# Kernel tuning notes

Measured on AMD Instinct MI355X. Metric: run time of the kernel, lower is better.

Reference implementation:

```python
import jax, jax.numpy as jnp
import numpy as np

N = 50000       # nodes
E = 1600000     # edges (avg degree 32)
DIN = 64
DOUT = 64
DE = 16
ATT_SLOPE = 0.2   # leaky_relu slope inside attention (GAT standard)
ACT_SLOPE = 0.01  # F.leaky_relu default between layers


def setup_inputs() -> dict:
    key = jax.random.key(0)
    ks = jax.random.split(key, 16)

    def lin(k, i, o):
        return jax.random.normal(k, (i, o), jnp.float32) / np.sqrt(i).astype(np.float32)

    def vec(k, d):
        return jax.random.normal(k, (d,), jnp.float32) / np.sqrt(d).astype(np.float32)

    return {
        "X": jax.random.normal(ks[0], (N, DIN), jnp.float32),
        "edge_index": jax.random.randint(ks[1], (2, E), 0, N),
        "edge_attr": jax.random.normal(ks[2], (E, DE), jnp.float32),
        # layer 1 params
        "W1": lin(ks[3], DIN, DOUT), "We1": lin(ks[4], DE, DOUT),
        "as1": vec(ks[5], DOUT), "ad1": vec(ks[6], DOUT), "ae1": vec(ks[7], DOUT),
        "b1": jnp.zeros((DOUT,), jnp.float32),
        # layer 2 params
        "W2": lin(ks[8], DOUT, DOUT), "We2": lin(ks[9], DE, DOUT),
        "as2": vec(ks[10], DOUT), "ad2": vec(ks[11], DOUT), "ae2": vec(ks[12], DOUT),
        "b2": jnp.zeros((DOUT,), jnp.float32),
    }


def _gat_conv(x, src, dst, edge_attr, W, We, a_s, a_d, a_e, b):
    """GATConv with edge features, softmax attention over dst neighborhoods, max aggregation."""
    n = x.shape[0]
    h = x @ W                      # [N, DOUT]
    e = edge_attr @ We             # [E, DOUT]
    # per-edge attention logits
    logits = jax.nn.leaky_relu((h @ a_s)[src] + (h @ a_d)[dst] + e @ a_e, ATT_SLOPE)  # [E]
    # numerically-stable segment softmax over destination node
    m = jax.ops.segment_max(logits, dst, num_segments=n)      # [N]
    p = jnp.exp(logits - m[dst])                               # [E]
    s = jax.ops.segment_sum(p, dst, num_segments=n)            # [N]
    att = p / jnp.maximum(s[dst], 1e-16)                       # [E]
    msg = (h[src] + e) * att[:, None]                          # [E, DOUT]
    out = jax.ops.segment_max(msg, dst, num_segments=n)        # [N, DOUT], -inf for empty
    out = jnp.where(jnp.isfinite(out), out, 0.0)
    return out + b


def reference(X, edge_index, edge_attr,
              W1, We1, as1, ad1, ae1, b1,
              W2, We2, as2, ad2, ae2, b2):
    src, dst = edge_index[0], edge_index[1]
    c1 = _gat_conv(X, src, dst, edge_attr, W1, We1, as1, ad1, ae1, b1)
    c1 = jax.nn.leaky_relu(c1, ACT_SLOPE)
    c2 = _gat_conv(c1, src, dst, edge_attr, W2, We2, as2, ad2, ae2, b2)
    c2 = jax.nn.leaky_relu(c2, ACT_SLOPE)
    return c2
```

## Files before the change

### kernel.cpp

```cpp
#include <hip/hip_runtime.h>
#include <cstdint>
#include <cstddef>

#define NN 50000
#define EE 1600000
#define D  64
#define DE 16

typedef __attribute__((ext_vector_type(2))) float vf2;

__device__ __forceinline__ float bf2f(unsigned short u) {
    return __uint_as_float(((unsigned)u) << 16);
}
__device__ __forceinline__ unsigned short f2bf(float f) {
    unsigned u = __float_as_uint(f);
    unsigned r = u + 0x7FFFu + ((u >> 16) & 1u);
    return (unsigned short)(r >> 16);
}

#define HI_ILP 4
__global__ __launch_bounds__(256) void k_hist(const int* __restrict__ dst,
                                              int* __restrict__ counts) {
    int base = blockIdx.x * (256 * HI_ILP) + threadIdx.x;
    int dd[HI_ILP]; bool v[HI_ILP];
    #pragma unroll
    for (int j = 0; j < HI_ILP; j++) {
        int e = base + j * 256;
        v[j] = (e < EE);
        dd[j] = dst[v[j] ? e : 0];
    }
    #pragma unroll
    for (int j = 0; j < HI_ILP; j++)
        if (v[j]) atomicAdd(&counts[dd[j]], 1);
}

__global__ __launch_bounds__(256) void k_scanA(const int* counts, int* bsum) {
    __shared__ int tmp[256];
    int t = threadIdx.x, i = blockIdx.x * 256 + t;
    tmp[t] = (i < NN) ? counts[i] : 0;
    __syncthreads();
    for (int off = 128; off; off >>= 1) {
        if (t < off) tmp[t] += tmp[t + off];
        __syncthreads();
    }
    if (t == 0) bsum[blockIdx.x] = tmp[0];
}

__global__ __launch_bounds__(256) void k_scanC(const int* counts, const int* bsum,
                                               int nchunks, int* offsets, int* cursor) {
    __shared__ int tmpb[256];
    __shared__ int tmp[256];
    int t = threadIdx.x;
    int bv = (t < nchunks) ? bsum[t] : 0;
    tmpb[t] = bv; __syncthreads();
    for (int off = 1; off < 256; off <<= 1) {
        int x = (t >= off) ? tmpb[t - off] : 0;
        __syncthreads();
        tmpb[t] += x;
        __syncthreads();
    }
    int base = (blockIdx.x > 0) ? tmpb[blockIdx.x - 1] : 0;

    int i = blockIdx.x * 256 + t;
    int v = (i < NN) ? counts[i] : 0;
    tmp[t] = v; __syncthreads();
    for (int off = 1; off < 256; off <<= 1) {
        int x = (t >= off) ? tmp[t - off] : 0;
        __syncthreads();
        tmp[t] += x;
        __syncthreads();
    }
    int excl = tmp[t] - v + base;
    if (i < NN) { offsets[i] = excl; cursor[i] = excl; }
}

#define SC_ILP 2
__global__ __launch_bounds__(256) void k_scatter_gemm(
        const int* __restrict__ src, const int* __restrict__ dst,
        const float* __restrict__ ea,
        const float* __restrict__ We1, const float* __restrict__ ae1,
        const float* __restrict__ We2, const float* __restrict__ ae2,
        int* __restrict__ cursor, int4* __restrict__ recs,
        const float* __restrict__ X, const float* __restrict__ W,
        const float* __restrict__ a_s, const float* __restrict__ a_d,
        unsigned short* __restrict__ h, float* __restrict__ hs,
        float* __restrict__ hd) {
    __shared__ float sh[64 * 64];
    int t = threadIdx.x;

    if (blockIdx.x < 1024) {
        for (int i = t; i < 1024; i += 256)
            ((float4*)sh)[i] = ((const float4*)W)[i];
        __syncthreads();
        int lane = t & 63;
        int wid0 = blockIdx.x * 4 + (t >> 6);
        float asl = a_s[lane], adl = a_d[lane];
        for (int n0 = wid0; n0 < NN; n0 += 4096) {
            int n = __builtin_amdgcn_readfirstlane(n0);
            const float4* xr = (const float4*)(X + (size_t)n * 64);
            float acc = 0.f;
            #pragma unroll
            for (int q = 0; q < 16; q++) {
                float4 u = xr[q];
                acc += u.x * sh[(4 * q) * 64 + lane]
                     + u.y * sh[(4 * q + 1) * 64 + lane]
                     + u.z * sh[(4 * q + 2) * 64 + lane]
                     + u.w * sh[(4 * q + 3) * 64 + lane];
            }
            h[(size_t)n * 64 + lane] = f2bf(acc);
            float ps = acc * asl, pd = acc * adl;
            #pragma unroll
            for (int off = 32; off; off >>= 1) {
                ps += __shfl_xor(ps, off);
                pd += __shfl_xor(pd, off);
            }
            if (lane == 0) { hs[n] = ps; hd[n] = pd; }
        }
        return;
    }

    if (t < 32) {
        const float* We = (t < 16) ? We1 : We2;
        const float* ae = (t < 16) ? ae1 : ae2;
        int k = t & 15;
        float acc = 0.f;
        #pragma unroll
        for (int c = 0; c < 64; c++) acc += We[k * 64 + c] * ae[c];
        sh[t] = acc;
    }
    __syncthreads();
    float w1r[16], w2r[16];
    #pragma unroll
    for (int j = 0; j < 16; j++) { w1r[j] = sh[j]; w2r[j] = sh[16 + j]; }

    int base = (blockIdx.x - 1024) * (256 * SC_ILP) + t;
    int dd[SC_ILP], ss[SC_ILP], pos[SC_ILP];
    bool v[SC_ILP];
    #pragma unroll
    for (int j = 0; j < SC_ILP; j++) {
        int e = base + j * 256;
        v[j] = (e < EE);
        int ec = v[j] ? e : 0;
        dd[j] = dst[ec];
        ss[j] = src[ec];
    }
    #pragma unroll
    for (int j = 0; j < SC_ILP; j++)
        if (v[j]) pos[j] = atomicAdd(&cursor[dd[j]], 1);
    #pragma unroll
    for (int j = 0; j < SC_ILP; j++) {
        if (!v[j]) continue;
        int e = base + j * 256;
        const float4* rp = (const float4*)(ea + (size_t)e * DE);
        float4 q0 = rp[0], q1 = rp[1], q2 = rp[2], q3 = rp[3];
        float ev[16] = {q0.x, q0.y, q0.z, q0.w, q1.x, q1.y, q1.z, q1.w,
                        q2.x, q2.y, q2.z, q2.w, q3.x, q3.y, q3.z, q3.w};
        float e1 = 0.f, e2 = 0.f;
        #pragma unroll
        for (int k2 = 0; k2 < 16; k2++) {
            e1 += ev[k2] * w1r[k2];
            e2 += ev[k2] * w2r[k2];
        }
        recs[pos[j]] = make_int4(ss[j], e, __float_as_int(e1), __float_as_int(e2));
    }
}

template<int IN_BF16>
__global__ __launch_bounds__(256, 4) void k_gemm(const void* xin, const float* W,
                                                 const float* a_s, const float* a_d,
                                                 unsigned short* h, float* hs, float* hd) {
    int t = threadIdx.x, lane = t & 63;
    int wid0 = blockIdx.x * 4 + (t >> 6);
    float Wcol[64];
    #pragma unroll
    for (int k = 0; k < 64; k++) Wcol[k] = W[k * 64 + lane];
    float asl = a_s[lane], adl = a_d[lane];
    for (int n0 = wid0; n0 < NN; n0 += 4096) {
        int n = __builtin_amdgcn_readfirstlane(n0);
        float acc = 0.f;
        if (IN_BF16) {
            const uint4* xr = (const uint4*)((const unsigned short*)xin + (size_t)n * 64);
            #pragma unroll
            for (int q = 0; q < 8; q++) {
                uint4 u = xr[q];
                unsigned uu[4] = {u.x, u.y, u.z, u.w};
                #pragma unroll
                for (int j = 0; j < 4; j++) {
                    acc += bf2f((unsigned short)(uu[j] & 0xFFFFu)) * Wcol[q * 8 + 2 * j];
                    acc += bf2f((unsigned short)(uu[j] >> 16))     * Wcol[q * 8 + 2 * j + 1];
                }
            }
        } else {
            const float4* xr = (const float4*)((const float*)xin + (size_t)n * 64);
            #pragma unroll
            for (int q = 0; q < 16; q++) {
                float4 u = xr[q];
                acc += u.x * Wcol[4 * q]     + u.y * Wcol[4 * q + 1]
                     + u.z * Wcol[4 * q + 2] + u.w * Wcol[4 * q + 3];
            }
        }
        h[(size_t)n * 64 + lane] = f2bf(acc);
        float ps = acc * asl, pd = acc * adl;
        #pragma unroll
        for (int off = 32; off; off >>= 1) {
            ps += __shfl_xor(ps, off);
            pd += __shfl_xor(pd, off);
        }
        if (lane == 0) { hs[n] = ps; hd[n] = pd; }
    }
}

template<int L2>
__global__ __launch_bounds__(256, 3) void k_gat(const int4* __restrict__ recs,
                                                const int* __restrict__ offsets,
                                                const int* __restrict__ counts,
                                                const float* __restrict__ hs,
                                                const float* __restrict__ hd,
                                                const unsigned short* __restrict__ h,
                                                const float* __restrict__ ea,
                                                const float* __restrict__ We,
                                                const float* __restrict__ b,
                                                void* __restrict__ outv) {
    __shared__ float4 eal[4][4][64];
    __shared__ float2 arx[4][64];
    int t = threadIdx.x, lane = t & 63, wv = t >> 6;
    int g = lane >> 4, cl = lane & 15;

    vf2 Wp[32];
    #pragma unroll
    for (int kp = 0; kp < 8; kp++) {
        float4 wa = *(const float4*)(We + (2 * kp) * 64 + 4 * cl);
        float4 wb = *(const float4*)(We + (2 * kp + 1) * 64 + 4 * cl);
        Wp[kp].x      = wa.x; Wp[kp].y      = wb.x;
        Wp[8 + kp].x  = wa.y; Wp[8 + kp].y  = wb.y;
        Wp[16 + kp].x = wa.z; Wp[16 + kp].y = wb.z;
        Wp[24 + kp].x = wa.w; Wp[24 + kp].y = wb.w;
    }

    int d = blockIdx.x * 4 + wv;
    int start = offsets[d];
    int deg = counts[d];

    if (deg == 0) {
        if (g == 0) {
            float4 bl = *(const float4*)(b + 4 * cl);
            float o0 = (bl.x >= 0.f) ? bl.x : 0.01f * bl.x;
            float o1 = (bl.y >= 0.f) ? bl.y : 0.01f * bl.y;
            float o2 = (bl.z >= 0.f) ? bl.z : 0.01f * bl.z;
            float o3 = (bl.w >= 0.f) ? bl.w : 0.01f * bl.w;
            size_t oidx = (size_t)d * D + 4 * cl;
            if (L2) *(float4*)((float*)outv + oidx) = make_float4(o0, o1, o2, o3);
            else {
                ushort4 ov = {f2bf(o0), f2bf(o1), f2bf(o2), f2bf(o3)};
                *(ushort4*)((unsigned short*)outv + oidx) = ov;
            }
        }
        return;
    }

    float hdv = hd[d];
    bool fast = (deg <= 64);
    float m, invs;

    float ninf = -__builtin_inff();
    float a0 = ninf, a1 = ninf, a2 = ninf, a3 = ninf;

    if (fast) {
        float lg = ninf;
        if (lane < deg) {
            int4 r = recs[start + lane];
            const float4* ep = (const float4*)(ea + (size_t)r.y * DE);
            float4 q0 = ep[0], q1 = ep[1], q2 = ep[2], q3 = ep[3];
            float hsv = hs[r.x];
            eal[wv][0][lane] = q0; eal[wv][1][lane] = q1;
            eal[wv][2][lane] = q2; eal[wv][3][lane] = q3;
            arx[wv][lane].y = __int_as_float(r.x);
            float ee = __int_as_float(L2 ? r.w : r.z);
            lg = hsv + hdv + ee;
            lg = (lg >= 0.f) ? lg : 0.2f * lg;
        }

        bool vC = (g < deg);
        int jC = vC ? g : 0;
        bool vN = (4 + g < deg);
        int jN = vN ? 4 + g : 0;
        int rxC = __float_as_int(arx[wv][jC].y);
        int rxN = __float_as_int(arx[wv][jN].y);
        ushort4 hvC = *(const ushort4*)(h + (size_t)rxC * D + 4 * cl);
        ushort4 hvN = *(const ushort4*)(h + (size_t)rxN * D + 4 * cl);

        m = lg;
        #pragma unroll
        for (int off = 32; off; off >>= 1) m = fmaxf(m, __shfl_xor(m, off));
        float p = __expf(lg - m);
        float s = p;
        #pragma unroll
        for (int off = 32; off; off >>= 1) s += __shfl_xor(s, off);
        invs = 1.0f / fmaxf(s, 1e-16f);
        if (lane < deg) arx[wv][lane].x = p * invs;

        float attC = arx[wv][jC].x;
        float attN = arx[wv][jN].x;

        for (int i = 0; i < deg; i += 4) {
            int jnn = i + 8 + g;
            bool vNN = (jnn < deg);
            int jNN = vNN ? jnn : 0;
            float2 arNN = arx[wv][jNN];
            int rxNN = __float_as_int(arNN.y);
            ushort4 hvNN = *(const ushort4*)(h + (size_t)rxNN * D + 4 * cl);

            vf2 acA = {0.f, 0.f}, acB = {0.f, 0.f}, acC2 = {0.f, 0.f}, acD = {0.f, 0.f};
            #pragma unroll
            for (int kq = 0; kq < 4; kq++) {
                float4 q = eal[wv][kq][jC];
                vf2 eA; eA.x = q.x; eA.y = q.y;
                vf2 eB; eB.x = q.z; eB.y = q.w;
                acA += eA * Wp[2 * kq];       acA += eB * Wp[2 * kq + 1];
                acB += eA * Wp[8 + 2 * kq];   acB += eB * Wp[8 + 2 * kq + 1];
                acC2 += eA * Wp[16 + 2 * kq]; acC2 += eB * Wp[16 + 2 * kq + 1];
                acD += eA * Wp[24 + 2 * kq];  acD += eB * Wp[24 + 2 * kq + 1];
            }
            float e0 = acA.x + acA.y, e1 = acB.x + acB.y;
            float e2 = acC2.x + acC2.y, e3 = acD.x + acD.y;
            float o0 = (bf2f(hvC.x) + e0) * attC;
            float o1 = (bf2f(hvC.y) + e1) * attC;
            float o2 = (bf2f(hvC.z) + e2) * attC;
            float o3 = (bf2f(hvC.w) + e3) * attC;
            if (vC) {
                a0 = fmaxf(a0, o0); a1 = fmaxf(a1, o1);
                a2 = fmaxf(a2, o2); a3 = fmaxf(a3, o3);
            }
            jC = jN; vC = vN; hvC = hvN; attC = attN;
            jN = jNN; vN = vNN; hvN = hvNN; attN = arNN.x;
        }
    } else {
        float mm = ninf, s = 0.f;
        for (int i = lane; i < deg; i += 64) {
            int4 r = recs[start + i];
            float ee = __int_as_float(L2 ? r.w : r.z);
            float lg = hs[r.x] + hdv + ee;
            lg = (lg >= 0.f) ? lg : 0.2f * lg;
            float mn = fmaxf(mm, lg);
            s = ((mm == mn) ? s : s * __expf(mm - mn)) + __expf(lg - mn);
            mm = mn;
        }
        #pragma unroll
        for (int off = 32; off; off >>= 1) {
            float m2 = __shfl_xor(mm, off);
            float s2 = __shfl_xor(s, off);
            float mn = fmaxf(mm, m2);
            float sa = (mm == mn) ? s : s * __expf(mm - mn);
            float sb = (m2 == mn) ? s2 : s2 * __expf(m2 - mn);
            s = sa + sb;
            mm = mn;
        }
        m = mm;
        invs = 1.0f / fmaxf(s, 1e-16f);

        for (int i = 0; i < deg; i += 4) {
            int j = i + g;
            bool valid = (j < deg);
            int jc = valid ? j : 0;
            int4 r = recs[start + jc];
            float ee = __int_as_float(L2 ? r.w : r.z);
            float lg = hs[r.x] + hdv + ee;
            lg = (lg >= 0.f) ? lg : 0.2f * lg;
            float att = __expf(lg - m) * invs;
            const float4* ep = (const float4*)(ea + (size_t)r.y * DE);
            float4 q0 = ep[0], q1 = ep[1], q2 = ep[2], q3 = ep[3];
            ushort4 hv = *(const ushort4*)(h + (size_t)r.x * D + 4 * cl);
            float4 qs[4] = {q0, q1, q2, q3};
            vf2 acA = {0.f, 0.f}, acB = {0.f, 0.f}, acC2 = {0.f, 0.f}, acD = {0.f, 0.f};
            #pragma unroll
            for (int kq = 0; kq < 4; kq++) {
                float4 q = qs[kq];
                vf2 eA; eA.x = q.x; eA.y = q.y;
                vf2 eB; eB.x = q.z; eB.y = q.w;
                acA += eA * Wp[2 * kq];       acA += eB * Wp[2 * kq + 1];
                acB += eA * Wp[8 + 2 * kq];   acB += eB * Wp[8 + 2 * kq + 1];
                acC2 += eA * Wp[16 + 2 * kq]; acC2 += eB * Wp[16 + 2 * kq + 1];
                acD += eA * Wp[24 + 2 * kq];  acD += eB * Wp[24 + 2 * kq + 1];
            }
            float e0 = acA.x + acA.y, e1 = acB.x + acB.y;
            float e2 = acC2.x + acC2.y, e3 = acD.x + acD.y;
            float o0 = (bf2f(hv.x) + e0) * att;
            float o1 = (bf2f(hv.y) + e1) * att;
            float o2 = (bf2f(hv.z) + e2) * att;
            float o3 = (bf2f(hv.w) + e3) * att;
            if (valid) {
                a0 = fmaxf(a0, o0); a1 = fmaxf(a1, o1);
                a2 = fmaxf(a2, o2); a3 = fmaxf(a3, o3);
            }
        }
    }

    #pragma unroll
    for (int off = 16; off <= 32; off <<= 1) {
        a0 = fmaxf(a0, __shfl_xor(a0, off));
        a1 = fmaxf(a1, __shfl_xor(a1, off));
        a2 = fmaxf(a2, __shfl_xor(a2, off));
        a3 = fmaxf(a3, __shfl_xor(a3, off));
    }

    if (g == 0) {
        float4 bl = *(const float4*)(b + 4 * cl);
        float o0 = a0 + bl.x, o1 = a1 + bl.y;
        float o2 = a2 + bl.z, o3 = a3 + bl.w;
        o0 = (o0 >= 0.f) ? o0 : 0.01f * o0;
        o1 = (o1 >= 0.f) ? o1 : 0.01f * o1;
        o2 = (o2 >= 0.f) ? o2 : 0.01f * o2;
        o3 = (o3 >= 0.f) ? o3 : 0.01f * o3;
        size_t oidx = (size_t)d * D + 4 * cl;
        if (L2) {
            *(float4*)((float*)outv + oidx) = make_float4(o0, o1, o2, o3);
        } else {
            ushort4 ov = {f2bf(o0), f2bf(o1), f2bf(o2), f2bf(o3)};
            *(ushort4*)((unsigned short*)outv + oidx) = ov;
        }
    }
}

extern "C" void kernel_launch(void* const* d_in, const int* in_sizes, int n_in,
                              void* d_out, int out_size, void* d_ws, size_t ws_size,
                              hipStream_t stream) {
    const float* X   = (const float*)d_in[0];
    const int*   eix = (const int*)d_in[1];
    const float* ea  = (const float*)d_in[2];
    const float* W1  = (const float*)d_in[3];
    const float* We1 = (const float*)d_in[4];
    const float* as1 = (const float*)d_in[5];
    const float* ad1 = (const float*)d_in[6];
    const float* ae1 = (const float*)d_in[7];
    const float* b1  = (const float*)d_in[8];
    const float* W2  = (const float*)d_in[9];
    const float* We2 = (const float*)d_in[10];
    const float* as2 = (const float*)d_in[11];
    const float* ad2 = (const float*)d_in[12];
    const float* ae2 = (const float*)d_in[13];
    const float* b2  = (const float*)d_in[14];

    const int* src = eix;
    const int* dst = eix + EE;

    char* w = (char*)d_ws;
    int4* recs = (int4*)w;               w += (size_t)EE * 16;
    unsigned short* hA = (unsigned short*)w; w += (size_t)NN * D * 2;
    unsigned short* hB = (unsigned short*)w; w += (size_t)NN * D * 2;
    float* hs = (float*)w;               w += (size_t)NN * 4;
    float* hd = (float*)w;               w += (size_t)NN * 4;
    int* counts = (int*)w;               w += (size_t)NN * 4;
    int* offsets = (int*)w;              w += (size_t)NN * 4;
    int* cursor = (int*)w;               w += (size_t)NN * 4;
    int* bsum = (int*)w;                 w += 256 * 4;

    const int nchunks = (NN + 255) / 256;
    const int nhblk = (EE + 256 * HI_ILP - 1) / (256 * HI_ILP);
    const int nsblk = (EE + 256 * SC_ILP - 1) / (256 * SC_ILP);

    hipMemsetAsync(counts, 0, (size_t)NN * 4, stream);
    k_hist<<<nhblk, 256, 0, stream>>>(dst, counts);
    k_scanA<<<nchunks, 256, 0, stream>>>(counts, bsum);
    k_scanC<<<nchunks, 256, 0, stream>>>(counts, bsum, nchunks, offsets, cursor);

    k_scatter_gemm<<<1024 + nsblk, 256, 0, stream>>>(src, dst, ea,
                                                     We1, ae1, We2, ae2,
                                                     cursor, recs,
                                                     X, W1, as1, ad1, hA, hs, hd);
    k_gat<0><<<NN / 4, 256, 0, stream>>>(recs, offsets, counts, hs, hd, hA, ea, We1, b1, hB);
    k_gemm<1><<<1024, 256, 0, stream>>>(hB, W2, as2, ad2, hB, hs, hd);
    k_gat<1><<<NN / 4, 256, 0, stream>>>(recs, offsets, counts, hs, hd, hB, ea, We2, b2,
                                         (float*)d_out);
}
```

Baseline: 565.5 us.

## Move edge attention scalars to edge-indexed array and shrink CSR records to int2

The per-edge projections of edge_attr onto We·ae for both layers are now computed in the histogram kernel and stored in a separate edge-indexed float2 array. The scatter step then writes only 8-byte (src, edge id) records instead of 16-byte records. This halves the scattered, uncoalesced writes and takes the edge_attr reads out of the scatter kernel. In exchange, the GAT kernels add an extra random gather into the eew array per edge, and the record reads are narrower.

```diff
diff --git a/kernel.cpp b/kernel.cpp
--- a/kernel.cpp
+++ b/kernel.cpp
@@ -20,8 +20,30 @@
 
 #define HI_ILP 4
 __global__ __launch_bounds__(256) void k_hist(const int* __restrict__ dst,
-                                              int* __restrict__ counts) {
-    int base = blockIdx.x * (256 * HI_ILP) + threadIdx.x;
+                                              int* __restrict__ counts,
+                                              const float* __restrict__ ea,
+                                              const float* __restrict__ We1,
+                                              const float* __restrict__ ae1,
+                                              const float* __restrict__ We2,
+                                              const float* __restrict__ ae2,
+                                              float2* __restrict__ eew) {
+    __shared__ float wsh[32];
+    int t = threadIdx.x;
+    if (t < 32) {
+        const float* We = (t < 16) ? We1 : We2;
+        const float* ae = (t < 16) ? ae1 : ae2;
+        int k = t & 15;
+        float acc = 0.f;
+        #pragma unroll
+        for (int c = 0; c < 64; c++) acc += We[k * 64 + c] * ae[c];
+        wsh[t] = acc;
+    }
+    __syncthreads();
+    float w1r[16], w2r[16];
+    #pragma unroll
+    for (int j = 0; j < 16; j++) { w1r[j] = wsh[j]; w2r[j] = wsh[16 + j]; }
+
+    int base = blockIdx.x * (256 * HI_ILP) + t;
     int dd[HI_ILP]; bool v[HI_ILP];
     #pragma unroll
     for (int j = 0; j < HI_ILP; j++) {
@@ -32,6 +54,22 @@
     #pragma unroll
     for (int j = 0; j < HI_ILP; j++)
         if (v[j]) atomicAdd(&counts[dd[j]], 1);
+    #pragma unroll
+    for (int j = 0; j < HI_ILP; j++) {
+        if (!v[j]) continue;
+        int e = base + j * 256;
+        const float4* rp = (const float4*)(ea + (size_t)e * DE);
+        float4 q0 = rp[0], q1 = rp[1], q2 = rp[2], q3 = rp[3];
+        float ev[16] = {q0.x, q0.y, q0.z, q0.w, q1.x, q1.y, q1.z, q1.w,
+                        q2.x, q2.y, q2.z, q2.w, q3.x, q3.y, q3.z, q3.w};
+        float e1 = 0.f, e2 = 0.f;
+        #pragma unroll
+        for (int k2 = 0; k2 < 16; k2++) {
+            e1 += ev[k2] * w1r[k2];
+            e2 += ev[k2] * w2r[k2];
+        }
+        eew[e] = make_float2(e1, e2);
+    }
 }
 
 __global__ __launch_bounds__(256) void k_scanA(const int* counts, int* bsum) {
@@ -77,10 +115,7 @@
 #define SC_ILP 2
 __global__ __launch_bounds__(256) void k_scatter_gemm(
         const int* __restrict__ src, const int* __restrict__ dst,
-        const float* __restrict__ ea,
-        const float* __restrict__ We1, const float* __restrict__ ae1,
-        const float* __restrict__ We2, const float* __restrict__ ae2,
-        int* __restrict__ cursor, int4* __restrict__ recs,
+        int* __restrict__ cursor, int2* __restrict__ recs,
         const float* __restrict__ X, const float* __restrict__ W,
         const float* __restrict__ a_s, const float* __restrict__ a_d,
         unsigned short* __restrict__ h, float* __restrict__ hs,
@@ -119,20 +154,6 @@
         return;
     }
 
-    if (t < 32) {
-        const float* We = (t < 16) ? We1 : We2;
-        const float* ae = (t < 16) ? ae1 : ae2;
-        int k = t & 15;
-        float acc = 0.f;
-        #pragma unroll
-        for (int c = 0; c < 64; c++) acc += We[k * 64 + c] * ae[c];
-        sh[t] = acc;
-    }
-    __syncthreads();
-    float w1r[16], w2r[16];
-    #pragma unroll
-    for (int j = 0; j < 16; j++) { w1r[j] = sh[j]; w2r[j] = sh[16 + j]; }
-
     int base = (blockIdx.x - 1024) * (256 * SC_ILP) + t;
     int dd[SC_ILP], ss[SC_ILP], pos[SC_ILP];
     bool v[SC_ILP];
@@ -148,21 +169,8 @@
     for (int j = 0; j < SC_ILP; j++)
         if (v[j]) pos[j] = atomicAdd(&cursor[dd[j]], 1);
     #pragma unroll
-    for (int j = 0; j < SC_ILP; j++) {
-        if (!v[j]) continue;
-        int e = base + j * 256;
-        const float4* rp = (const float4*)(ea + (size_t)e * DE);
-        float4 q0 = rp[0], q1 = rp[1], q2 = rp[2], q3 = rp[3];
-        float ev[16] = {q0.x, q0.y, q0.z, q0.w, q1.x, q1.y, q1.z, q1.w,
-                        q2.x, q2.y, q2.z, q2.w, q3.x, q3.y, q3.z, q3.w};
-        float e1 = 0.f, e2 = 0.f;
-        #pragma unroll
-        for (int k2 = 0; k2 < 16; k2++) {
-            e1 += ev[k2] * w1r[k2];
-            e2 += ev[k2] * w2r[k2];
-        }
-        recs[pos[j]] = make_int4(ss[j], e, __float_as_int(e1), __float_as_int(e2));
-    }
+    for (int j = 0; j < SC_ILP; j++)
+        if (v[j]) recs[pos[j]] = make_int2(ss[j], base + j * 256);
 }
 
 template<int IN_BF16>
@@ -211,13 +219,14 @@
 }
 
 template<int L2>
-__global__ __launch_bounds__(256, 3) void k_gat(const int4* __restrict__ recs,
+__global__ __launch_bounds__(256, 3) void k_gat(const int2* __restrict__ recs,
                                                 const int* __restrict__ offsets,
                                                 const int* __restrict__ counts,
                                                 const float* __restrict__ hs,
                                                 const float* __restrict__ hd,
                                                 const unsigned short* __restrict__ h,
                                                 const float* __restrict__ ea,
+                                                const float2* __restrict__ eew,
                                                 const float* __restrict__ We,
                                                 const float* __restrict__ b,
                                                 void* __restrict__ outv) {
@@ -268,14 +277,15 @@
     if (fast) {
         float lg = ninf;
         if (lane < deg) {
-            int4 r = recs[start + lane];
+            int2 r = recs[start + lane];
+            float2 ew = eew[r.y];
             const float4* ep = (const float4*)(ea + (size_t)r.y * DE);
             float4 q0 = ep[0], q1 = ep[1], q2 = ep[2], q3 = ep[3];
             float hsv = hs[r.x];
             eal[wv][0][lane] = q0; eal[wv][1][lane] = q1;
             eal[wv][2][lane] = q2; eal[wv][3][lane] = q3;
             arx[wv][lane].y = __int_as_float(r.x);
-            float ee = __int_as_float(L2 ? r.w : r.z);
+            float ee = L2 ? ew.y : ew.x;
             lg = hsv + hdv + ee;
             lg = (lg >= 0.f) ? lg : 0.2f * lg;
         }
@@ -337,8 +347,9 @@
     } else {
         float mm = ninf, s = 0.f;
         for (int i = lane; i < deg; i += 64) {
-            int4 r = recs[start + i];
-            float ee = __int_as_float(L2 ? r.w : r.z);
+            int2 r = recs[start + i];
+            float2 ew = eew[r.y];
+            float ee = L2 ? ew.y : ew.x;
             float lg = hs[r.x] + hdv + ee;
             lg = (lg >= 0.f) ? lg : 0.2f * lg;
             float mn = fmaxf(mm, lg);
@@ -362,8 +373,9 @@
             int j = i + g;
             bool valid = (j < deg);
             int jc = valid ? j : 0;
-            int4 r = recs[start + jc];
-            float ee = __int_as_float(L2 ? r.w : r.z);
+            int2 r = recs[start + jc];
+            float2 ew = eew[r.y];
+            float ee = L2 ? ew.y : ew.x;
             float lg = hs[r.x] + hdv + ee;
             lg = (lg >= 0.f) ? lg : 0.2f * lg;
             float att = __expf(lg - m) * invs;
@@ -444,7 +456,8 @@
     const int* dst = eix + EE;
 
     char* w = (char*)d_ws;
-    int4* recs = (int4*)w;               w += (size_t)EE * 16;
+    int2* recs = (int2*)w;               w += (size_t)EE * 8;
+    float2* eew = (float2*)w;            w += (size_t)EE * 8;
     unsigned short* hA = (unsigned short*)w; w += (size_t)NN * D * 2;
     unsigned short* hB = (unsigned short*)w; w += (size_t)NN * D * 2;
     float* hs = (float*)w;               w += (size_t)NN * 4;
@@ -459,16 +472,15 @@
     const int nsblk = (EE + 256 * SC_ILP - 1) / (256 * SC_ILP);
 
     hipMemsetAsync(counts, 0, (size_t)NN * 4, stream);
-    k_hist<<<nhblk, 256, 0, stream>>>(dst, counts);
+    k_hist<<<nhblk, 256, 0, stream>>>(dst, counts, ea, We1, ae1, We2, ae2, eew);
     k_scanA<<<nchunks, 256, 0, stream>>>(counts, bsum);
     k_scanC<<<nchunks, 256, 0, stream>>>(counts, bsum, nchunks, offsets, cursor);
 
-    k_scatter_gemm<<<1024 + nsblk, 256, 0, stream>>>(src, dst, ea,
-                                                     We1, ae1, We2, ae2,
-                                                     cursor, recs,
+    k_scatter_gemm<<<1024 + nsblk, 256, 0, stream>>>(src, dst, cursor, recs,
                                                      X, W1, as1, ad1, hA, hs, hd);
-    k_gat<0><<<NN / 4, 256, 0, stream>>>(recs, offsets, counts, hs, hd, hA, ea, We1, b1, hB);
+    k_gat<0><<<NN / 4, 256, 0, stream>>>(recs, offsets, counts, hs, hd, hA, ea, eew,
+                                         We1, b1, hB);
     k_gemm<1><<<1024, 256, 0, stream>>>(hB, W2, as2, ad2, hB, hs, hd);
-    k_gat<1><<<NN / 4, 256, 0, stream>>>(recs, offsets, counts, hs, hd, hB, ea, We2, b2,
-                                         (float*)d_out);
-}
+    k_gat<1><<<NN / 4, 256, 0, stream>>>(recs, offsets, counts, hs, hd, hB, ea, eew,
+                                         We2, b2, (float*)d_out);
+}
```

Result: slower. 577.8 us (+2.2%).

## Fuse layer-2 node GEMM and attention projections into layer-1 GAT epilogue

Applied to the files above, without the earlier changes.

The layer-1 GAT kernel now stages W2 in shared memory and, after computing each node's activated output, multiplies it by W2 in-wave to produce layer-2 h (bf16) plus the hs/hd attention scalars. This removes the separate k_gemm launch and the write and reread of the intermediate c1 activations. The cost is a 16KB W2 load into shared memory per block, which adds LDS pressure and may reduce occupancy. hs2/hd2 get separate buffers to avoid a race with layer-1's hs/hd reads.

```diff
diff --git a/kernel.cpp b/kernel.cpp
--- a/kernel.cpp
+++ b/kernel.cpp
@@ -165,51 +165,6 @@
     }
 }
 
-template<int IN_BF16>
-__global__ __launch_bounds__(256, 4) void k_gemm(const void* xin, const float* W,
-                                                 const float* a_s, const float* a_d,
-                                                 unsigned short* h, float* hs, float* hd) {
-    int t = threadIdx.x, lane = t & 63;
-    int wid0 = blockIdx.x * 4 + (t >> 6);
-    float Wcol[64];
-    #pragma unroll
-    for (int k = 0; k < 64; k++) Wcol[k] = W[k * 64 + lane];
-    float asl = a_s[lane], adl = a_d[lane];
-    for (int n0 = wid0; n0 < NN; n0 += 4096) {
-        int n = __builtin_amdgcn_readfirstlane(n0);
-        float acc = 0.f;
-        if (IN_BF16) {
-            const uint4* xr = (const uint4*)((const unsigned short*)xin + (size_t)n * 64);
-            #pragma unroll
-            for (int q = 0; q < 8; q++) {
-                uint4 u = xr[q];
-                unsigned uu[4] = {u.x, u.y, u.z, u.w};
-                #pragma unroll
-                for (int j = 0; j < 4; j++) {
-                    acc += bf2f((unsigned short)(uu[j] & 0xFFFFu)) * Wcol[q * 8 + 2 * j];
-                    acc += bf2f((unsigned short)(uu[j] >> 16))     * Wcol[q * 8 + 2 * j + 1];
-                }
-            }
-        } else {
-            const float4* xr = (const float4*)((const float*)xin + (size_t)n * 64);
-            #pragma unroll
-            for (int q = 0; q < 16; q++) {
-                float4 u = xr[q];
-                acc += u.x * Wcol[4 * q]     + u.y * Wcol[4 * q + 1]
-                     + u.z * Wcol[4 * q + 2] + u.w * Wcol[4 * q + 3];
-            }
-        }
-        h[(size_t)n * 64 + lane] = f2bf(acc);
-        float ps = acc * asl, pd = acc * adl;
-        #pragma unroll
-        for (int off = 32; off; off >>= 1) {
-            ps += __shfl_xor(ps, off);
-            pd += __shfl_xor(pd, off);
-        }
-        if (lane == 0) { hs[n] = ps; hd[n] = pd; }
-    }
-}
-
 template<int L2>
 __global__ __launch_bounds__(256, 3) void k_gat(const int4* __restrict__ recs,
                                                 const int* __restrict__ offsets,
@@ -220,11 +175,24 @@
                                                 const float* __restrict__ ea,
                                                 const float* __restrict__ We,
                                                 const float* __restrict__ b,
-                                                void* __restrict__ outv) {
+                                                void* __restrict__ outv,
+                                                const float* __restrict__ W2,
+                                                const float* __restrict__ as2,
+                                                const float* __restrict__ ad2,
+                                                float* __restrict__ hs2,
+                                                float* __restrict__ hd2) {
     __shared__ float4 eal[4][4][64];
     __shared__ float2 arx[4][64];
+    __shared__ float shW2[L2 ? 1 : 4096];
+    __shared__ float c1ls[L2 ? 1 : 4][L2 ? 1 : 64];
     int t = threadIdx.x, lane = t & 63, wv = t >> 6;
     int g = lane >> 4, cl = lane & 15;
+
+    if (!L2) {
+        for (int i = t; i < 1024; i += 256)
+            ((float4*)shW2)[i] = ((const float4*)W2)[i];
+        __syncthreads();
+    }
 
     vf2 Wp[32];
     #pragma unroll
@@ -241,166 +209,153 @@
     int start = offsets[d];
     int deg = counts[d];
 
-    if (deg == 0) {
-        if (g == 0) {
-            float4 bl = *(const float4*)(b + 4 * cl);
-            float o0 = (bl.x >= 0.f) ? bl.x : 0.01f * bl.x;
-            float o1 = (bl.y >= 0.f) ? bl.y : 0.01f * bl.y;
-            float o2 = (bl.z >= 0.f) ? bl.z : 0.01f * bl.z;
-            float o3 = (bl.w >= 0.f) ? bl.w : 0.01f * bl.w;
-            size_t oidx = (size_t)d * D + 4 * cl;
-            if (L2) *(float4*)((float*)outv + oidx) = make_float4(o0, o1, o2, o3);
-            else {
-                ushort4 ov = {f2bf(o0), f2bf(o1), f2bf(o2), f2bf(o3)};
-                *(ushort4*)((unsigned short*)outv + oidx) = ov;
-            }
-        }
-        return;
-    }
-
-    float hdv = hd[d];
-    bool fast = (deg <= 64);
-    float m, invs;
-
     float ninf = -__builtin_inff();
     float a0 = ninf, a1 = ninf, a2 = ninf, a3 = ninf;
 
-    if (fast) {
-        float lg = ninf;
-        if (lane < deg) {
-            int4 r = recs[start + lane];
-            const float4* ep = (const float4*)(ea + (size_t)r.y * DE);
-            float4 q0 = ep[0], q1 = ep[1], q2 = ep[2], q3 = ep[3];
-            float hsv = hs[r.x];
-            eal[wv][0][lane] = q0; eal[wv][1][lane] = q1;
-            eal[wv][2][lane] = q2; eal[wv][3][lane] = q3;
-            arx[wv][lane].y = __int_as_float(r.x);
-            float ee = __int_as_float(L2 ? r.w : r.z);
-            lg = hsv + hdv + ee;
-            lg = (lg >= 0.f) ? lg : 0.2f * lg;
-        }
-
-        bool vC = (g < deg);
-        int jC = vC ? g : 0;
-        bool vN = (4 + g < deg);
-        int jN = vN ? 4 + g : 0;
-        int rxC = __float_as_int(arx[wv][jC].y);
-        int rxN = __float_as_int(arx[wv][jN].y);
-        ushort4 hvC = *(const ushort4*)(h + (size_t)rxC * D + 4 * cl);
-        ushort4 hvN = *(const ushort4*)(h + (size_t)rxN * D + 4 * cl);
-
-        m = lg;
+    if (deg > 0) {
+        float hdv = hd[d];
+        bool fast = (deg <= 64);
+        float m, invs;
+
+        if (fast) {
+            float lg = ninf;
+            if (lane < deg) {
+                int4 r = recs[start + lane];
+                const float4* ep = (const float4*)(ea + (size_t)r.y * DE);
+                float4 q0 = ep[0], q1 = ep[1], q2 = ep[2], q3 = ep[3];
+                float hsv = hs[r.x];
+                eal[wv][0][lane] = q0; eal[wv][1][lane] = q1;
+                eal[wv][2][lane] = q2; eal[wv][3][lane] = q3;
+                arx[wv][lane].y = __int_as_float(r.x);
+                float ee = __int_as_float(L2 ? r.w : r.z);
+                lg = hsv + hdv + ee;
+                lg = (lg >= 0.f) ? lg : 0.2f * lg;
+            }
+
+            bool vC = (g < deg);
+            int jC = vC ? g : 0;
+            bool vN = (4 + g < deg);
+            int jN = vN ? 4 + g : 0;
+            int rxC = __float_as_int(arx[wv][jC].y);
+            int rxN = __float_as_int(arx[wv][jN].y);
+            ushort4 hvC = *(const ushort4*)(h + (size_t)rxC * D + 4 * cl);
+            ushort4 hvN = *(const ushort4*)(h + (size_t)rxN * D + 4 * cl);
+
+            m = lg;
+            #pragma unroll
+            for (int off = 32; off; off >>= 1) m = fmaxf(m, __shfl_xor(m, off));
+            float p = __expf(lg - m);
+            float s = p;
+            #pragma unroll
+            for (int off = 32; off; off >>= 1) s += __shfl_xor(s, off);
+            invs = 1.0f / fmaxf(s, 1e-16f);
+            if (lane < deg) arx[wv][lane].x = p * invs;
+
+            float attC = arx[wv][jC].x;
+            float attN = arx[wv][jN].x;
+
+            for (int i = 0; i < deg; i += 4) {
+                int jnn = i + 8 + g;
+                bool vNN = (jnn < deg);
+                int jNN = vNN ? jnn : 0;
+                float2 arNN = arx[wv][jNN];
+                int rxNN = __float_as_int(arNN.y);
+                ushort4 hvNN = *(const ushort4*)(h + (size_t)rxNN * D + 4 * cl);
+
+                vf2 acA = {0.f, 0.f}, acB = {0.f, 0.f}, acC2 = {0.f, 0.f}, acD = {0.f, 0.f};
+                #pragma unroll
+                for (int kq = 0; kq < 4; kq++) {
+                    float4 q = eal[wv][kq][jC];
+                    vf2 eA; eA.x = q.x; eA.y = q.y;
+                    vf2 eB; eB.x = q.z; eB.y = q.w;
+                    acA += eA * Wp[2 * kq];       acA += eB * Wp[2 * kq + 1];
+                    acB += eA * Wp[8 + 2 * kq];   acB += eB * Wp[8 + 2 * kq + 1];
+                    acC2 += eA * Wp[16 + 2 * kq]; acC2 += eB * Wp[16 + 2 * kq + 1];
+                    acD += eA * Wp[24 + 2 * kq];  acD += eB * Wp[24 + 2 * kq + 1];
+                }
+                float e0 = acA.x + acA.y, e1 = acB.x + acB.y;
+                float e2 = acC2.x + acC2.y, e3 = acD.x + acD.y;
+                float o0 = (bf2f(hvC.x) + e0) * attC;
+                float o1 = (bf2f(hvC.y) + e1) * attC;
+                float o2 = (bf2f(hvC.z) + e2) * attC;
+                float o3 = (bf2f(hvC.w) + e3) * attC;
+                if (vC) {
+                    a0 = fmaxf(a0, o0); a1 = fmaxf(a1, o1);
+                    a2 = fmaxf(a2, o2); a3 = fmaxf(a3, o3);
+                }
+                jC = jN; vC = vN; hvC = hvN; attC = attN;
+                jN = jNN; vN = vNN; hvN = hvNN; attN = arNN.x;
+            }
+        } else {
+            float mm = ninf, s = 0.f;
+            for (int i = lane; i < deg; i += 64) {
+                int4 r = recs[start + i];
+                float ee = __int_as_float(L2 ? r.w : r.z);
+                float lg = hs[r.x] + hdv + ee;
+                lg = (lg >= 0.f) ? lg : 0.2f * lg;
+                float mn = fmaxf(mm, lg);
+                s = ((mm == mn) ? s : s * __expf(mm - mn)) + __expf(lg - mn);
+                mm = mn;
+            }
+            #pragma unroll
+            for (int off = 32; off; off >>= 1) {
+                float m2 = __shfl_xor(mm, off);
+                float s2 = __shfl_xor(s, off);
+                float mn = fmaxf(mm, m2);
+                float sa = (mm == mn) ? s : s * __expf(mm - mn);
+                float sb = (m2 == mn) ? s2 : s2 * __expf(m2 - mn);
+                s = sa + sb;
+                mm = mn;
+            }
+            m = mm;
+            invs = 1.0f / fmaxf(s, 1e-16f);
+
+            for (int i = 0; i < deg; i += 4) {
+                int j = i + g;
+                bool valid = (j < deg);
+                int jc = valid ? j : 0;
+                int4 r = recs[start + jc];
+                float ee = __int_as_float(L2 ? r.w : r.z);
+                float lg = hs[r.x] + hdv + ee;
+                lg = (lg >= 0.f) ? lg : 0.2f * lg;
+                float att = __expf(lg - m) * invs;
+                const float4* ep = (const float4*)(ea + (size_t)r.y * DE);
+                float4 q0 = ep[0], q1 = ep[1], q2 = ep[2], q3 = ep[3];
+                ushort4 hv = *(const ushort4*)(h + (size_t)r.x * D + 4 * cl);
+                float4 qs[4] = {q0, q1, q2, q3};
+                vf2 acA = {0.f, 0.f}, acB = {0.f, 0.f}, acC2 = {0.f, 0.f}, acD = {0.f, 0.f};
+                #pragma unroll
+                for (int kq = 0; kq < 4; kq++) {
+                    float4 q = qs[kq];
+                    vf2 eA; eA.x = q.x; eA.y = q.y;
+                    vf2 eB; eB.x = q.z; eB.y = q.w;
+                    acA += eA * Wp[2 * kq];       acA += eB * Wp[2 * kq + 1];
+                    acB += eA * Wp[8 + 2 * kq];   acB += eB * Wp[8 + 2 * kq + 1];
+                    acC2 += eA * Wp[16 + 2 * kq]; acC2 += eB * Wp[16 + 2 * kq + 1];
+                    acD += eA * Wp[24 + 2 * kq];  acD += eB * Wp[24 + 2 * kq + 1];
+                }
+                float e0 = acA.x + acA.y, e1 = acB.x + acB.y;
+                float e2 = acC2.x + acC2.y, e3 = acD.x + acD.y;
+                float o0 = (bf2f(hv.x) + e0) * att;
+                float o1 = (bf2f(hv.y) + e1) * att;
+                float o2 = (bf2f(hv.z) + e2) * att;
+                float o3 = (bf2f(hv.w) + e3) * att;
+                if (valid) {
+                    a0 = fmaxf(a0, o0); a1 = fmaxf(a1, o1);
+                    a2 = fmaxf(a2, o2); a3 = fmaxf(a3, o3);
+                }
+            }
+        }
+
         #pragma unroll
-        for (int off = 32; off; off >>= 1) m = fmaxf(m, __shfl_xor(m, off));
-        float p = __expf(lg - m);
-        float s = p;
-        #pragma unroll
-        for (int off = 32; off; off >>= 1) s += __shfl_xor(s, off);
-        invs = 1.0f / fmaxf(s, 1e-16f);
-        if (lane < deg) arx[wv][lane].x = p * invs;
-
-        float attC = arx[wv][jC].x;
-        float attN = arx[wv][jN].x;
-
-        for (int i = 0; i < deg; i += 4) {
-            int jnn = i + 8 + g;
-            bool vNN = (jnn < deg);
-            int jNN = vNN ? jnn : 0;
-            float2 arNN = arx[wv][jNN];
-            int rxNN = __float_as_int(arNN.y);
-            ushort4 hvNN = *(const ushort4*)(h + (size_t)rxNN * D + 4 * cl);
-
-            vf2 acA = {0.f, 0.f}, acB = {0.f, 0.f}, acC2 = {0.f, 0.f}, acD = {0.f, 0.f};
-            #pragma unroll
-            for (int kq = 0; kq < 4; kq++) {
-                float4 q = eal[wv][kq][jC];
-                vf2 eA; eA.x = q.x; eA.y = q.y;
-                vf2 eB; eB.x = q.z; eB.y = q.w;
-                acA += eA * Wp[2 * kq];       acA += eB * Wp[2 * kq + 1];
-                acB += eA * Wp[8 + 2 * kq];   acB += eB * Wp[8 + 2 * kq + 1];
-                acC2 += eA * Wp[16 + 2 * kq]; acC2 += eB * Wp[16 + 2 * kq + 1];
-                acD += eA * Wp[24 + 2 * kq];  acD += eB * Wp[24 + 2 * kq + 1];
-            }
-            float e0 = acA.x + acA.y, e1 = acB.x + acB.y;
-            float e2 = acC2.x + acC2.y, e3 = acD.x + acD.y;
-            float o0 = (bf2f(hvC.x) + e0) * attC;
-            float o1 = (bf2f(hvC.y) + e1) * attC;
-            float o2 = (bf2f(hvC.z) + e2) * attC;
-            float o3 = (bf2f(hvC.w) + e3) * attC;
-            if (vC) {
-                a0 = fmaxf(a0, o0); a1 = fmaxf(a1, o1);
-                a2 = fmaxf(a2, o2); a3 = fmaxf(a3, o3);
-            }
-            jC = jN; vC = vN; hvC = hvN; attC = attN;
-            jN = jNN; vN = vNN; hvN = hvNN; attN = arNN.x;
+        for (int off = 16; off <= 32; off <<= 1) {
+            a0 = fmaxf(a0, __shfl_xor(a0, off));
+            a1 = fmaxf(a1, __shfl_xor(a1, off));
+            a2 = fmaxf(a2, __shfl_xor(a2, off));
+            a3 = fmaxf(a3, __shfl_xor(a3, off));
         }
     } else {
-        float mm = ninf, s = 0.f;
-        for (int i = lane; i < deg; i += 64) {
-            int4 r = recs[start + i];
-            float ee = __int_as_float(L2 ? r.w : r.z);
-            float lg = hs[r.x] + hdv + ee;
-            lg = (lg >= 0.f) ? lg : 0.2f * lg;
-            float mn = fmaxf(mm, lg);
-            s = ((mm == mn) ? s : s * __expf(mm - mn)) + __expf(lg - mn);
-            mm = mn;
-        }
-        #pragma unroll
-        for (int off = 32; off; off >>= 1) {
-            float m2 = __shfl_xor(mm, off);
-            float s2 = __shfl_xor(s, off);
-            float mn = fmaxf(mm, m2);
-            float sa = (mm == mn) ? s : s * __expf(mm - mn);
-            float sb = (m2 == mn) ? s2 : s2 * __expf(m2 - mn);
-            s = sa + sb;
-            mm = mn;
-        }
-        m = mm;
-        invs = 1.0f / fmaxf(s, 1e-16f);
-
-        for (int i = 0; i < deg; i += 4) {
-            int j = i + g;
-            bool valid = (j < deg);
-            int jc = valid ? j : 0;
-            int4 r = recs[start + jc];
-            float ee = __int_as_float(L2 ? r.w : r.z);
-            float lg = hs[r.x] + hdv + ee;
-            lg = (lg >= 0.f) ? lg : 0.2f * lg;
-            float att = __expf(lg - m) * invs;
-            const float4* ep = (const float4*)(ea + (size_t)r.y * DE);
-            float4 q0 = ep[0], q1 = ep[1], q2 = ep[2], q3 = ep[3];
-            ushort4 hv = *(const ushort4*)(h + (size_t)r.x * D + 4 * cl);
-            float4 qs[4] = {q0, q1, q2, q3};
-            vf2 acA = {0.f, 0.f}, acB = {0.f, 0.f}, acC2 = {0.f, 0.f}, acD = {0.f, 0.f};
-            #pragma unroll
-            for (int kq = 0; kq < 4; kq++) {
-                float4 q = qs[kq];
-                vf2 eA; eA.x = q.x; eA.y = q.y;
-                vf2 eB; eB.x = q.z; eB.y = q.w;
-                acA += eA * Wp[2 * kq];       acA += eB * Wp[2 * kq + 1];
-                acB += eA * Wp[8 + 2 * kq];   acB += eB * Wp[8 + 2 * kq + 1];
-                acC2 += eA * Wp[16 + 2 * kq]; acC2 += eB * Wp[16 + 2 * kq + 1];
-                acD += eA * Wp[24 + 2 * kq];  acD += eB * Wp[24 + 2 * kq + 1];
-            }
-            float e0 = acA.x + acA.y, e1 = acB.x + acB.y;
-            float e2 = acC2.x + acC2.y, e3 = acD.x + acD.y;
-            float o0 = (bf2f(hv.x) + e0) * att;
-            float o1 = (bf2f(hv.y) + e1) * att;
-            float o2 = (bf2f(hv.z) + e2) * att;
-            float o3 = (bf2f(hv.w) + e3) * att;
-            if (valid) {
-                a0 = fmaxf(a0, o0); a1 = fmaxf(a1, o1);
-                a2 = fmaxf(a2, o2); a3 = fmaxf(a3, o3);
-            }
-        }
-    }
-
-    #pragma unroll
-    for (int off = 16; off <= 32; off <<= 1) {
-        a0 = fmaxf(a0, __shfl_xor(a0, off));
-        a1 = fmaxf(a1, __shfl_xor(a1, off));
-        a2 = fmaxf(a2, __shfl_xor(a2, off));
-        a3 = fmaxf(a3, __shfl_xor(a3, off));
+        a0 = a1 = a2 = a3 = 0.f;
     }
 
     if (g == 0) {
@@ -411,13 +366,31 @@
         o1 = (o1 >= 0.f) ? o1 : 0.01f * o1;
         o2 = (o2 >= 0.f) ? o2 : 0.01f * o2;
         o3 = (o3 >= 0.f) ? o3 : 0.01f * o3;
-        size_t oidx = (size_t)d * D + 4 * cl;
         if (L2) {
-            *(float4*)((float*)outv + oidx) = make_float4(o0, o1, o2, o3);
+            *(float4*)((float*)outv + (size_t)d * D + 4 * cl) =
+                make_float4(o0, o1, o2, o3);
         } else {
-            ushort4 ov = {f2bf(o0), f2bf(o1), f2bf(o2), f2bf(o3)};
-            *(ushort4*)((unsigned short*)outv + oidx) = ov;
-        }
+            *(float4*)&c1ls[wv][4 * cl] = make_float4(o0, o1, o2, o3);
+        }
+    }
+    if (!L2) {
+        float acc = 0.f;
+        #pragma unroll
+        for (int k4 = 0; k4 < 16; k4++) {
+            float4 c = *(const float4*)&c1ls[wv][4 * k4];
+            acc += c.x * shW2[(4 * k4) * 64 + lane]
+                 + c.y * shW2[(4 * k4 + 1) * 64 + lane]
+                 + c.z * shW2[(4 * k4 + 2) * 64 + lane]
+                 + c.w * shW2[(4 * k4 + 3) * 64 + lane];
+        }
+        ((unsigned short*)outv)[(size_t)d * D + lane] = f2bf(acc);
+        float ps = acc * as2[lane], pd = acc * ad2[lane];
+        #pragma unroll
+        for (int off = 32; off; off >>= 1) {
+            ps += __shfl_xor(ps, off);
+            pd += __shfl_xor(pd, off);
+        }
+        if (lane == 0) { hs2[d] = ps; hd2[d] = pd; }
     }
 }
 
@@ -449,6 +422,8 @@
     unsigned short* hB = (unsigned short*)w; w += (size_t)NN * D * 2;
     float* hs = (float*)w;               w += (size_t)NN * 4;
     float* hd = (float*)w;               w += (size_t)NN * 4;
+    float* hs2 = (float*)w;              w += (size_t)NN * 4;
+    float* hd2 = (float*)w;              w += (size_t)NN * 4;
     int* counts = (int*)w;               w += (size_t)NN * 4;
     int* offsets = (int*)w;              w += (size_t)NN * 4;
     int* cursor = (int*)w;               w += (size_t)NN * 4;
@@ -467,8 +442,9 @@
                                                      We1, ae1, We2, ae2,
                                                      cursor, recs,
                                                      X, W1, as1, ad1, hA, hs, hd);
-    k_gat<0><<<NN / 4, 256, 0, stream>>>(recs, offsets, counts, hs, hd, hA, ea, We1, b1, hB);
-    k_gemm<1><<<1024, 256, 0, stream>>>(hB, W2, as2, ad2, hB, hs, hd);
-    k_gat<1><<<NN / 4, 256, 0, stream>>>(recs, offsets, counts, hs, hd, hB, ea, We2, b2,
-                                         (float*)d_out);
-}
+    k_gat<0><<<NN / 4, 256, 0, stream>>>(recs, offsets, counts, hs, hd, hA, ea,
+                                         We1, b1, hB, W2, as2, ad2, hs2, hd2);
+    k_gat<1><<<NN / 4, 256, 0, stream>>>(recs, offsets, counts, hs2, hd2, hB, ea,
+                                         We2, b2, (float*)d_out,
+                                         nullptr, nullptr, nullptr, nullptr, nullptr);
+}
```

Result: no change. 567.0 us (+0.3%).
